# Kernel optimization log

Hardware: AMD Instinct MI355X
Metric: run time of the kernel (lower is better)

## Reference

```python
import jax, jax.numpy as jnp
import numpy as np

# Shapes: n groups, l = max group length, d = d_h, N = total queries (nq.sum()).
N_Q, N_GRP, L, D = 4096, 256, 64, 512


def setup_inputs() -> dict:
    key = jax.random.key(0)
    ks = jax.random.split(key, 8)
    q = jax.random.normal(ks[0], (N_Q, 2 * D), dtype=jnp.float32)      # cat([h_src, h_dst])
    k = jax.random.normal(ks[1], (N_GRP, L, D), dtype=jnp.float32)      # h_grp
    v = jax.random.normal(ks[2], (N_GRP, L, D), dtype=jnp.float32)      # x_grp
    m = (jax.random.uniform(ks[3], (N_GRP, L)) > 0.2).astype(jnp.float32)
    # sorted group id per query == repeat_interleave(arange(n), nq)
    gid = jnp.sort(jax.random.randint(ks[4], (N_Q,), 0, N_GRP))
    Wq = jax.random.normal(ks[5], (2 * D, D), dtype=jnp.float32) / np.float32(np.sqrt(2 * D))
    bq = jnp.zeros((D,), dtype=jnp.float32)
    Wk = jax.random.normal(ks[6], (D, D), dtype=jnp.float32) / np.float32(np.sqrt(D))
    bk = jnp.zeros((D,), dtype=jnp.float32)
    return dict(q=q, k=k, v=v, m=m, gid=gid, Wq=Wq, bq=bq, Wk=Wk, bk=bk)


def reference(q, k, v, m, gid, Wq, bq, Wk, bk):
    """Faithful jax version of NounPhraseModel.attention.

    torch: q -> self.q(q); k -> self.k(k); repeat_interleave(nq, 0) on k/v/m;
    s = (k @ q) / sqrt(d) - (exp(50*(1-m)) - 1); out = (v * softmax(s, 1)).sum(1).
    repeat_interleave is expressed as a gather by the per-query group id `gid`.
    """
    d = k.shape[-1]
    qp = q @ Wq + bq                                   # (N, d)   self.q(q)
    kp = k @ Wk + bk                                   # (n, l, d) self.k(k)
    kg = kp[gid]                                       # (N, l, d)
    vg = v[gid]                                        # (N, l, d)
    mg = m[gid]                                        # (N, l)
    s = jnp.einsum('nd,nld->nl', qp, kg) / jnp.sqrt(jnp.float32(d))
    s = s - (jnp.exp(50.0 * (1.0 - mg)) - 1.0)         # exponential mask bias
    a = jax.nn.softmax(s, axis=1)                      # softmax over group length
    return jnp.einsum('nl,nld->nd', a, vg)             # (N, d)
```

## Files before the change

### kernel.cpp

```cpp
#include <hip/hip_runtime.h>

#define NQ   4096
#define NGRP 256
#define LL   64
#define DD   512

typedef __attribute__((ext_vector_type(8))) short short8v;
typedef __attribute__((ext_vector_type(4))) float f32x4;
typedef __attribute__((ext_vector_type(4))) unsigned short us4v;

#define SCALE 0.044194173824159216f

static __device__ __forceinline__ unsigned short f2bf(float f) {
  union { float f; unsigned u; } x{f};
  unsigned r = x.u + 0x7fffu + ((x.u >> 16) & 1u);
  return (unsigned short)(r >> 16);
}
static __device__ __forceinline__ float bf2f(unsigned short h) {
  union { unsigned u; float f; } x{(unsigned)h << 16};
  return x.f;
}

static __device__ __forceinline__ void split_store(
    unsigned short* Hh, unsigned short* Hl, int r, int c4, float4 v) {
  int s = c4 >> 1, hf = c4 & 1;
  int base = (r * 8 + (s ^ (r & 7))) * 8 + hf * 4;
  unsigned short h0 = f2bf(v.x), h1 = f2bf(v.y), h2 = f2bf(v.z), h3 = f2bf(v.w);
  us4v hv = {h0, h1, h2, h3};
  us4v lv = {f2bf(v.x - bf2f(h0)), f2bf(v.y - bf2f(h1)),
             f2bf(v.z - bf2f(h2)), f2bf(v.w - bf2f(h3))};
  *(us4v*)(Hh + base) = hv;
  *(us4v*)(Hl + base) = lv;
}

static __device__ __forceinline__ short8v frag(const unsigned short* P, int r, int sl) {
  return *(const short8v*)(P + (r * 8 + (sl ^ (r & 7))) * 8);
}

__global__ __launch_bounds__(256) void k_prep(
    const float* __restrict__ q_in, const int* __restrict__ gid,
    const float* __restrict__ Wk, const float* __restrict__ Wq,
    const float* __restrict__ bq,
    unsigned short* __restrict__ qbf, int* __restrict__ starts,
    float* __restrict__ b2,
    unsigned short* __restrict__ w2t_h, unsigned short* __restrict__ w2t_l) {
  __shared__ __align__(16) unsigned short lds[4 * 64 * 64];
  int b = blockIdx.x, t = threadIdx.x;
  if (b < 128) {
    unsigned short* Ah = lds;
    unsigned short* Al = lds + 4096;
    unsigned short* Bh = lds + 8192;
    unsigned short* Bl = lds + 12288;
    int lane = t & 63, wid = t >> 6;
    int wm = wid >> 1, wn = wid & 1;
    int n0 = (b & 15) * 64, m0 = (b >> 4) * 64;
    f32x4 acc[2][2];
    #pragma unroll
    for (int i = 0; i < 2; ++i)
      #pragma unroll
      for (int j = 0; j < 2; ++j) acc[i][j] = (f32x4){0.f,0.f,0.f,0.f};

    for (int k0 = 0; k0 < 512; k0 += 64) {
      __syncthreads();
      #pragma unroll
      for (int i = 0; i < 4; ++i) {
        int idx = i * 256 + t, r = idx >> 4, c4 = idx & 15;
        float4 vA = *(const float4*)&Wk[(size_t)(m0 + r) * 512 + k0 + c4 * 4];
        split_store(Ah, Al, r, c4, vA);
        float4 vB = *(const float4*)&Wq[(size_t)(n0 + r) * 512 + k0 + c4 * 4];
        split_store(Bh, Bl, r, c4, vB);
      }
      __syncthreads();
      #pragma unroll
      for (int kk = 0; kk < 2; ++kk) {
        int sl = kk * 4 + (lane >> 4);
        short8v aH[2], aL[2], bH[2], bL[2];
        #pragma unroll
        for (int fm = 0; fm < 2; ++fm) {
          int r = wm * 32 + fm * 16 + (lane & 15);
          aH[fm] = frag(Ah, r, sl); aL[fm] = frag(Al, r, sl);
        }
        #pragma unroll
        for (int fn = 0; fn < 2; ++fn) {
          int r = wn * 32 + fn * 16 + (lane & 15);
          bH[fn] = frag(Bh, r, sl); bL[fn] = frag(Bl, r, sl);
        }
        #pragma unroll
        for (int fm = 0; fm < 2; ++fm)
          #pragma unroll
          for (int fn = 0; fn < 2; ++fn) {
            acc[fm][fn] = __builtin_amdgcn_mfma_f32_16x16x32_bf16(aH[fm], bH[fn], acc[fm][fn], 0, 0, 0);
            acc[fm][fn] = __builtin_amdgcn_mfma_f32_16x16x32_bf16(aH[fm], bL[fn], acc[fm][fn], 0, 0, 0);
            acc[fm][fn] = __builtin_amdgcn_mfma_f32_16x16x32_bf16(aL[fm], bH[fn], acc[fm][fn], 0, 0, 0);
          }
      }
    }
    int cn = lane & 15, rq = lane >> 4;
    #pragma unroll
    for (int fm = 0; fm < 2; ++fm)
      #pragma unroll
      for (int fn = 0; fn < 2; ++fn)
        #pragma unroll
        for (int j = 0; j < 4; ++j) {
          int m = m0 + wm * 32 + fm * 16 + rq * 4 + j;
          int n = n0 + wn * 32 + fn * 16 + cn;
          float c = acc[fm][fn][j];
          unsigned short hi = f2bf(c);
          unsigned short lo = f2bf(c - bf2f(hi));
          size_t off = (size_t)m * 1024 + n;
          w2t_h[off] = hi; w2t_l[off] = lo;
        }
  } else if (b < 2176) {
    int idx = (b - 128) * 256 + t;
    const float* src = q_in + (size_t)idx * 8;
    float4 f0 = *(const float4*)src;
    float4 f1 = *(const float4*)(src + 4);
    uint4 pk;
    pk.x = (unsigned)f2bf(f0.x) | ((unsigned)f2bf(f0.y) << 16);
    pk.y = (unsigned)f2bf(f0.z) | ((unsigned)f2bf(f0.w) << 16);
    pk.z = (unsigned)f2bf(f1.x) | ((unsigned)f2bf(f1.y) << 16);
    pk.w = (unsigned)f2bf(f1.z) | ((unsigned)f2bf(f1.w) << 16);
    ((uint4*)qbf)[idx] = pk;
  } else if (b == 2176) {
    for (int g = t; g <= NGRP; g += 256) {
      int lo = 0, hi = NQ;
      while (lo < hi) { int mid = (lo + hi) >> 1; if (gid[mid] < g) lo = mid + 1; else hi = mid; }
      starts[g] = lo;
    }
  } else {
    int dd = (b - 2177) * 256 + t;
    if (dd < DD) {
      float s = 0.f;
      const float* row = Wk + (size_t)dd * DD;
      for (int j = 0; j < DD; j += 4) {
        float4 w = *(const float4*)&row[j];
        float4 bb = *(const float4*)&bq[j];
        s += w.x*bb.x + w.y*bb.y + w.z*bb.z + w.w*bb.w;
      }
      b2[dd] = s;
    }
  }
}

__global__ __launch_bounds__(256) void gemm_qt_mfma(
    const unsigned short* __restrict__ qbf,
    const unsigned short* __restrict__ w2t_h,
    const unsigned short* __restrict__ w2t_l,
    const float* __restrict__ b2,
    unsigned short* __restrict__ qt_h, unsigned short* __restrict__ qt_l) {
  __shared__ __align__(16) unsigned short As[64 * 64];
  __shared__ __align__(16) unsigned short Bh[64 * 64];
  __shared__ __align__(16) unsigned short Bl[64 * 64];
  int t = threadIdx.x;
  int lane = t & 63, wid = t >> 6;
  int wm = wid >> 1, wn = wid & 1;
  int n0 = blockIdx.x * 64, m0 = blockIdx.y * 64;

  f32x4 acc[2][2];
  #pragma unroll
  for (int i = 0; i < 2; ++i)
    #pragma unroll
    for (int j = 0; j < 2; ++j) acc[i][j] = (f32x4){0.f, 0.f, 0.f, 0.f};

  for (int k0 = 0; k0 < 1024; k0 += 64) {
    __syncthreads();
    #pragma unroll
    for (int i = 0; i < 2; ++i) {
      int idx = i * 256 + t;
      int r = idx >> 3, s = idx & 7;
      int dst = r * 8 + (s ^ (r & 7));
      ((uint4*)As)[dst] = *(const uint4*)(qbf + (size_t)(m0 + r) * 1024 + k0 + s * 8);
    }
    #pragma unroll
    for (int i = 0; i < 2; ++i) {
      int idx = i * 256 + t;
      int r = idx >> 3, s = idx & 7;
      int dst = r * 8 + (s ^ (r & 7));
      ((uint4*)Bh)[dst] = *(const uint4*)(w2t_h + (size_t)(n0 + r) * 1024 + k0 + s * 8);
      ((uint4*)Bl)[dst] = *(const uint4*)(w2t_l + (size_t)(n0 + r) * 1024 + k0 + s * 8);
    }
    __syncthreads();
    #pragma unroll
    for (int kk = 0; kk < 2; ++kk) {
      short8v aF[2], bHF[2], bLF[2];
      int sl = kk * 4 + (lane >> 4);
      #pragma unroll
      for (int fm = 0; fm < 2; ++fm)
        aF[fm] = frag(As, wm * 32 + fm * 16 + (lane & 15), sl);
      #pragma unroll
      for (int fn = 0; fn < 2; ++fn) {
        int r = wn * 32 + fn * 16 + (lane & 15);
        bHF[fn] = frag(Bh, r, sl);
        bLF[fn] = frag(Bl, r, sl);
      }
      #pragma unroll
      for (int fm = 0; fm < 2; ++fm)
        #pragma unroll
        for (int fn = 0; fn < 2; ++fn) {
          acc[fm][fn] = __builtin_amdgcn_mfma_f32_16x16x32_bf16(aF[fm], bHF[fn], acc[fm][fn], 0, 0, 0);
          acc[fm][fn] = __builtin_amdgcn_mfma_f32_16x16x32_bf16(aF[fm], bLF[fn], acc[fm][fn], 0, 0, 0);
        }
    }
  }
  int cn = lane & 15, rq = lane >> 4;
  #pragma unroll
  for (int fn = 0; fn < 2; ++fn) {
    int n = n0 + wn * 32 + fn * 16 + cn;
    float bias = b2[n];
    #pragma unroll
    for (int fm = 0; fm < 2; ++fm)
      #pragma unroll
      for (int j = 0; j < 4; ++j) {
        int m = m0 + wm * 32 + fm * 16 + rq * 4 + j;
        float val = acc[fm][fn][j] + bias;
        unsigned short hi = f2bf(val);
        unsigned short lo = f2bf(val - bf2f(hi));
        qt_h[(size_t)m * 512 + n] = hi;
        qt_l[(size_t)m * 512 + n] = lo;
      }
  }
}

__global__ __launch_bounds__(256) void k_scores4(
    const unsigned short* __restrict__ qt_h, const unsigned short* __restrict__ qt_l,
    const float* __restrict__ kk_, const int* __restrict__ starts,
    float* __restrict__ s_part) {
  int g = blockIdx.x >> 2, dq = blockIdx.x & 3;
  int t = threadIdx.x, lane = t & 63, wl = t >> 6;
  int s0 = starts[g], s1 = starts[g + 1];
  if (s0 >= s1) return;

  __shared__ __align__(16) unsigned short Kh[64*64], Kl[64*64];
  __shared__ __align__(16) unsigned short Qh[32*64], Ql[32*64];

  float* sp = s_part + (size_t)dq * NQ * LL;

  for (int cs = s0; cs < s1; cs += 32) {
    int qc = min(32, s1 - cs);
    f32x4 acc[2];
    acc[0] = (f32x4){0.f,0.f,0.f,0.f};
    acc[1] = (f32x4){0.f,0.f,0.f,0.f};

    #pragma unroll
    for (int kt = 0; kt < 2; ++kt) {
      int k0 = dq * 128 + kt * 64;
      __syncthreads();
      #pragma unroll
      for (int i = 0; i < 4; ++i) {
        int idx = i * 256 + t, r = idx >> 4, c4 = idx & 15;
        float4 v = *(const float4*)&kk_[((size_t)g * LL + r) * DD + k0 + c4 * 4];
        split_store(Kh, Kl, r, c4, v);
      }
      {
        int r = t >> 3, s = t & 7;
        uint4 vh = make_uint4(0,0,0,0), vl = make_uint4(0,0,0,0);
        if (r < qc) {
          vh = *(const uint4*)&qt_h[(size_t)(cs + r) * DD + k0 + s * 8];
          vl = *(const uint4*)&qt_l[(size_t)(cs + r) * DD + k0 + s * 8];
        }
        int slot = r * 8 + (s ^ (r & 7));
        ((uint4*)Qh)[slot] = vh;
        ((uint4*)Ql)[slot] = vl;
      }
      __syncthreads();
      #pragma unroll
      for (int kk = 0; kk < 2; ++kk) {
        int sl = kk * 4 + (lane >> 4);
        int rA = wl * 16 + (lane & 15);
        short8v aH = frag(Kh, rA, sl), aL = frag(Kl, rA, sl);
        #pragma unroll
        for (int fn = 0; fn < 2; ++fn) {
          int rB = fn * 16 + (lane & 15);
          short8v bH = frag(Qh, rB, sl), bL = frag(Ql, rB, sl);
          acc[fn] = __builtin_amdgcn_mfma_f32_16x16x32_bf16(aH, bH, acc[fn], 0, 0, 0);
          acc[fn] = __builtin_amdgcn_mfma_f32_16x16x32_bf16(aH, bL, acc[fn], 0, 0, 0);
          acc[fn] = __builtin_amdgcn_mfma_f32_16x16x32_bf16(aL, bH, acc[fn], 0, 0, 0);
        }
      }
    }
    {
      int cq = lane & 15, rq = lane >> 4;
      #pragma unroll
      for (int fn = 0; fn < 2; ++fn) {
        int q = fn * 16 + cq;
        if (q < qc) {
          float* row = sp + (size_t)(cs + q) * LL;
          #pragma unroll
          for (int j = 0; j < 4; ++j)
            row[wl * 16 + rq * 4 + j] = acc[fn][j];
        }
      }
    }
  }
}

__global__ __launch_bounds__(256) void k_pv2(
    const float* __restrict__ s_part, const float* __restrict__ vv_,
    const float* __restrict__ msk, const int* __restrict__ starts,
    float* __restrict__ out) {
  int g = blockIdx.x >> 1, dh = blockIdx.x & 1;
  int t = threadIdx.x, lane = t & 63, wid = t >> 6;
  int s0 = starts[g], s1 = starts[g + 1];
  if (s0 >= s1) return;

  __shared__ __align__(16) float S_lds[32][68];
  __shared__ float bias_lds[LL];
  if (t < LL) bias_lds[t] = __expf(50.0f * (1.0f - msk[g * LL + t])) - 1.0f;

  const float* vb = vv_ + (size_t)g * LL * DD + dh * 256 + lane * 4;

  for (int cs = s0; cs < s1; cs += 32) {
    int qc = min(32, s1 - cs);
    __syncthreads();
    #pragma unroll
    for (int i = 0; i < 2; ++i) {
      int f = i * 256 + t;
      int q = f >> 4, l4 = f & 15;
      const float* p = s_part + (size_t)(cs + q) * LL + l4 * 4;
      float4 a0 = *(const float4*)p;
      float4 a1 = *(const float4*)(p + (size_t)NQ * LL);
      float4 a2 = *(const float4*)(p + (size_t)2 * NQ * LL);
      float4 a3 = *(const float4*)(p + (size_t)3 * NQ * LL);
      float4 r;
      r.x = (a0.x + a1.x + a2.x + a3.x) * SCALE - bias_lds[l4 * 4 + 0];
      r.y = (a0.y + a1.y + a2.y + a3.y) * SCALE - bias_lds[l4 * 4 + 1];
      r.z = (a0.z + a1.z + a2.z + a3.z) * SCALE - bias_lds[l4 * 4 + 2];
      r.w = (a0.w + a1.w + a2.w + a3.w) * SCALE - bias_lds[l4 * 4 + 3];
      *(float4*)&S_lds[q][l4 * 4] = r;
    }
    __syncthreads();
    {
      int q = t >> 3, i = t & 7;
      float4 x0 = *(const float4*)&S_lds[q][i * 8];
      float4 x1 = *(const float4*)&S_lds[q][i * 8 + 4];
      float mx = fmaxf(fmaxf(fmaxf(x0.x, x0.y), fmaxf(x0.z, x0.w)),
                       fmaxf(fmaxf(x1.x, x1.y), fmaxf(x1.z, x1.w)));
      #pragma unroll
      for (int off = 1; off < 8; off <<= 1) mx = fmaxf(mx, __shfl_xor(mx, off, 8));
      float e0 = __expf(x0.x - mx), e1 = __expf(x0.y - mx);
      float e2 = __expf(x0.z - mx), e3 = __expf(x0.w - mx);
      float e4 = __expf(x1.x - mx), e5 = __expf(x1.y - mx);
      float e6 = __expf(x1.z - mx), e7 = __expf(x1.w - mx);
      float sum = ((e0 + e1) + (e2 + e3)) + ((e4 + e5) + (e6 + e7));
      #pragma unroll
      for (int off = 1; off < 8; off <<= 1) sum += __shfl_xor(sum, off, 8);
      float inv = 1.0f / sum;
      *(float4*)&S_lds[q][i * 8]     = make_float4(e0 * inv, e1 * inv, e2 * inv, e3 * inv);
      *(float4*)&S_lds[q][i * 8 + 4] = make_float4(e4 * inv, e5 * inv, e6 * inv, e7 * inv);
    }
    __syncthreads();
    {
      float o[8][4];
      #pragma unroll
      for (int u = 0; u < 8; ++u)
        #pragma unroll
        for (int e = 0; e < 4; ++e) o[u][e] = 0.f;
      for (int l0 = 0; l0 < LL; l0 += 4) {
        float a_[8][4];
        #pragma unroll
        for (int u = 0; u < 8; ++u) {
          float4 av = *(const float4*)&S_lds[wid * 8 + u][l0];
          a_[u][0] = av.x; a_[u][1] = av.y; a_[u][2] = av.z; a_[u][3] = av.w;
        }
        #pragma unroll
        for (int e = 0; e < 4; ++e) {
          float4 vv = *(const float4*)&vb[(size_t)(l0 + e) * DD];
          #pragma unroll
          for (int u = 0; u < 8; ++u) {
            o[u][0] += a_[u][e] * vv.x;
            o[u][1] += a_[u][e] * vv.y;
            o[u][2] += a_[u][e] * vv.z;
            o[u][3] += a_[u][e] * vv.w;
          }
        }
      }
      #pragma unroll
      for (int u = 0; u < 8; ++u) {
        int q = wid * 8 + u;
        if (q < qc) {
          *(float4*)&out[(size_t)(cs + q) * DD + dh * 256 + lane * 4] =
              make_float4(o[u][0], o[u][1], o[u][2], o[u][3]);
        }
      }
    }
  }
}

extern "C" void kernel_launch(void* const* d_in, const int* in_sizes, int n_in,
                              void* d_out, int out_size, void* d_ws, size_t ws_size,
                              hipStream_t stream) {
  const float* q_in = (const float*)d_in[0];
  const float* k_in = (const float*)d_in[1];
  const float* v_in = (const float*)d_in[2];
  const float* m_in = (const float*)d_in[3];
  const int*   gid  = (const int*)d_in[4];
  const float* Wq   = (const float*)d_in[5];
  const float* bq   = (const float*)d_in[6];
  const float* Wk   = (const float*)d_in[7];
  float* out = (float*)d_out;

  unsigned short* w2t_h = (unsigned short*)d_ws;
  unsigned short* w2t_l = w2t_h + 512 * 1024;
  unsigned short* qt_h  = w2t_l + 512 * 1024;
  unsigned short* qt_l  = qt_h + 4096 * 512;
  unsigned short* qbf   = qt_l + 4096 * 512;
  float* b2 = (float*)(qbf + 4096 * 1024);
  int* starts = (int*)(b2 + 512);
  float* s_part = (float*)(starts + 512);

  k_prep<<<2179, 256, 0, stream>>>(q_in, gid, Wk, Wq, bq, qbf, starts, b2, w2t_h, w2t_l);
  gemm_qt_mfma<<<dim3(8, 64), 256, 0, stream>>>(qbf, w2t_h, w2t_l, b2, qt_h, qt_l);
  k_scores4<<<NGRP * 4, 256, 0, stream>>>(qt_h, qt_l, k_in, starts, s_part);
  k_pv2<<<NGRP * 2, 256, 0, stream>>>(s_part, v_in, m_in, starts, out);
}
```

Before: 70.27 us.

## Drop hi/lo bf16 split for fused weight and projected queries; retile weight GEMM

```diff
diff --git a/kernel.cpp b/kernel.cpp
--- a/kernel.cpp
+++ b/kernel.cpp
@@ -42,28 +42,24 @@
     const float* __restrict__ Wk, const float* __restrict__ Wq,
     const float* __restrict__ bq,
     unsigned short* __restrict__ qbf, int* __restrict__ starts,
-    float* __restrict__ b2,
-    unsigned short* __restrict__ w2t_h, unsigned short* __restrict__ w2t_l) {
-  __shared__ __align__(16) unsigned short lds[4 * 64 * 64];
+    float* __restrict__ b2, unsigned short* __restrict__ w2t) {
+  __shared__ __align__(16) unsigned short lds[4 * 32 * 64];
   int b = blockIdx.x, t = threadIdx.x;
-  if (b < 128) {
+  if (b < 512) {
     unsigned short* Ah = lds;
-    unsigned short* Al = lds + 4096;
-    unsigned short* Bh = lds + 8192;
-    unsigned short* Bl = lds + 12288;
+    unsigned short* Al = lds + 2048;
+    unsigned short* Bh = lds + 4096;
+    unsigned short* Bl = lds + 6144;
     int lane = t & 63, wid = t >> 6;
     int wm = wid >> 1, wn = wid & 1;
-    int n0 = (b & 15) * 64, m0 = (b >> 4) * 64;
-    f32x4 acc[2][2];
-    #pragma unroll
-    for (int i = 0; i < 2; ++i)
-      #pragma unroll
-      for (int j = 0; j < 2; ++j) acc[i][j] = (f32x4){0.f,0.f,0.f,0.f};
+    int m0 = (b >> 5) * 32;
+    int n0 = (b & 31) * 32;
+    f32x4 acc = (f32x4){0.f, 0.f, 0.f, 0.f};
 
     for (int k0 = 0; k0 < 512; k0 += 64) {
       __syncthreads();
       #pragma unroll
-      for (int i = 0; i < 4; ++i) {
+      for (int i = 0; i < 2; ++i) {
         int idx = i * 256 + t, r = idx >> 4, c4 = idx & 15;
         float4 vA = *(const float4*)&Wk[(size_t)(m0 + r) * 512 + k0 + c4 * 4];
         split_store(Ah, Al, r, c4, vA);
@@ -74,44 +70,24 @@
       #pragma unroll
       for (int kk = 0; kk < 2; ++kk) {
         int sl = kk * 4 + (lane >> 4);
-        short8v aH[2], aL[2], bH[2], bL[2];
-        #pragma unroll
-        for (int fm = 0; fm < 2; ++fm) {
-          int r = wm * 32 + fm * 16 + (lane & 15);
-          aH[fm] = frag(Ah, r, sl); aL[fm] = frag(Al, r, sl);
-        }
-        #pragma unroll
-        for (int fn = 0; fn < 2; ++fn) {
-          int r = wn * 32 + fn * 16 + (lane & 15);
-          bH[fn] = frag(Bh, r, sl); bL[fn] = frag(Bl, r, sl);
-        }
-        #pragma unroll
-        for (int fm = 0; fm < 2; ++fm)
-          #pragma unroll
-          for (int fn = 0; fn < 2; ++fn) {
-            acc[fm][fn] = __builtin_amdgcn_mfma_f32_16x16x32_bf16(aH[fm], bH[fn], acc[fm][fn], 0, 0, 0);
-            acc[fm][fn] = __builtin_amdgcn_mfma_f32_16x16x32_bf16(aH[fm], bL[fn], acc[fm][fn], 0, 0, 0);
-            acc[fm][fn] = __builtin_amdgcn_mfma_f32_16x16x32_bf16(aL[fm], bH[fn], acc[fm][fn], 0, 0, 0);
-          }
+        int rA = wm * 16 + (lane & 15);
+        int rB = wn * 16 + (lane & 15);
+        short8v aH = frag(Ah, rA, sl), aL = frag(Al, rA, sl);
+        short8v bH = frag(Bh, rB, sl), bL = frag(Bl, rB, sl);
+        acc = __builtin_amdgcn_mfma_f32_16x16x32_bf16(aH, bH, acc, 0, 0, 0);
+        acc = __builtin_amdgcn_mfma_f32_16x16x32_bf16(aH, bL, acc, 0, 0, 0);
+        acc = __builtin_amdgcn_mfma_f32_16x16x32_bf16(aL, bH, acc, 0, 0, 0);
       }
     }
     int cn = lane & 15, rq = lane >> 4;
     #pragma unroll
-    for (int fm = 0; fm < 2; ++fm)
-      #pragma unroll
-      for (int fn = 0; fn < 2; ++fn)
-        #pragma unroll
-        for (int j = 0; j < 4; ++j) {
-          int m = m0 + wm * 32 + fm * 16 + rq * 4 + j;
-          int n = n0 + wn * 32 + fn * 16 + cn;
-          float c = acc[fm][fn][j];
-          unsigned short hi = f2bf(c);
-          unsigned short lo = f2bf(c - bf2f(hi));
-          size_t off = (size_t)m * 1024 + n;
-          w2t_h[off] = hi; w2t_l[off] = lo;
-        }
-  } else if (b < 2176) {
-    int idx = (b - 128) * 256 + t;
+    for (int j = 0; j < 4; ++j) {
+      int m = m0 + wm * 16 + rq * 4 + j;
+      int n = n0 + wn * 16 + cn;
+      w2t[(size_t)m * 1024 + n] = f2bf(acc[j]);
+    }
+  } else if (b < 2560) {
+    int idx = (b - 512) * 256 + t;
     const float* src = q_in + (size_t)idx * 8;
     float4 f0 = *(const float4*)src;
     float4 f1 = *(const float4*)(src + 4);
@@ -121,14 +97,14 @@
     pk.z = (unsigned)f2bf(f1.x) | ((unsigned)f2bf(f1.y) << 16);
     pk.w = (unsigned)f2bf(f1.z) | ((unsigned)f2bf(f1.w) << 16);
     ((uint4*)qbf)[idx] = pk;
-  } else if (b == 2176) {
+  } else if (b == 2560) {
     for (int g = t; g <= NGRP; g += 256) {
       int lo = 0, hi = NQ;
       while (lo < hi) { int mid = (lo + hi) >> 1; if (gid[mid] < g) lo = mid + 1; else hi = mid; }
       starts[g] = lo;
     }
   } else {
-    int dd = (b - 2177) * 256 + t;
+    int dd = (b - 2561) * 256 + t;
     if (dd < DD) {
       float s = 0.f;
       const float* row = Wk + (size_t)dd * DD;
@@ -144,13 +120,11 @@
 
 __global__ __launch_bounds__(256) void gemm_qt_mfma(
     const unsigned short* __restrict__ qbf,
-    const unsigned short* __restrict__ w2t_h,
-    const unsigned short* __restrict__ w2t_l,
+    const unsigned short* __restrict__ w2t,
     const float* __restrict__ b2,
-    unsigned short* __restrict__ qt_h, unsigned short* __restrict__ qt_l) {
+    unsigned short* __restrict__ qt) {
   __shared__ __align__(16) unsigned short As[64 * 64];
-  __shared__ __align__(16) unsigned short Bh[64 * 64];
-  __shared__ __align__(16) unsigned short Bl[64 * 64];
+  __shared__ __align__(16) unsigned short Bs[64 * 64];
   int t = threadIdx.x;
   int lane = t & 63, wid = t >> 6;
   int wm = wid >> 1, wn = wid & 1;
@@ -170,36 +144,24 @@
       int r = idx >> 3, s = idx & 7;
       int dst = r * 8 + (s ^ (r & 7));
       ((uint4*)As)[dst] = *(const uint4*)(qbf + (size_t)(m0 + r) * 1024 + k0 + s * 8);
-    }
-    #pragma unroll
-    for (int i = 0; i < 2; ++i) {
-      int idx = i * 256 + t;
-      int r = idx >> 3, s = idx & 7;
-      int dst = r * 8 + (s ^ (r & 7));
-      ((uint4*)Bh)[dst] = *(const uint4*)(w2t_h + (size_t)(n0 + r) * 1024 + k0 + s * 8);
-      ((uint4*)Bl)[dst] = *(const uint4*)(w2t_l + (size_t)(n0 + r) * 1024 + k0 + s * 8);
+      ((uint4*)Bs)[dst] = *(const uint4*)(w2t + (size_t)(n0 + r) * 1024 + k0 + s * 8);
     }
     __syncthreads();
     #pragma unroll
     for (int kk = 0; kk < 2; ++kk) {
-      short8v aF[2], bHF[2], bLF[2];
+      short8v aF[2], bF[2];
       int sl = kk * 4 + (lane >> 4);
       #pragma unroll
       for (int fm = 0; fm < 2; ++fm)
         aF[fm] = frag(As, wm * 32 + fm * 16 + (lane & 15), sl);
       #pragma unroll
-      for (int fn = 0; fn < 2; ++fn) {
-        int r = wn * 32 + fn * 16 + (lane & 15);
-        bHF[fn] = frag(Bh, r, sl);
-        bLF[fn] = frag(Bl, r, sl);
-      }
+      for (int fn = 0; fn < 2; ++fn)
+        bF[fn] = frag(Bs, wn * 32 + fn * 16 + (lane & 15), sl);
       #pragma unroll
       for (int fm = 0; fm < 2; ++fm)
         #pragma unroll
-        for (int fn = 0; fn < 2; ++fn) {
-          acc[fm][fn] = __builtin_amdgcn_mfma_f32_16x16x32_bf16(aF[fm], bHF[fn], acc[fm][fn], 0, 0, 0);
-          acc[fm][fn] = __builtin_amdgcn_mfma_f32_16x16x32_bf16(aF[fm], bLF[fn], acc[fm][fn], 0, 0, 0);
-        }
+        for (int fn = 0; fn < 2; ++fn)
+          acc[fm][fn] = __builtin_amdgcn_mfma_f32_16x16x32_bf16(aF[fm], bF[fn], acc[fm][fn], 0, 0, 0);
     }
   }
   int cn = lane & 15, rq = lane >> 4;
@@ -212,17 +174,13 @@
       #pragma unroll
       for (int j = 0; j < 4; ++j) {
         int m = m0 + wm * 32 + fm * 16 + rq * 4 + j;
-        float val = acc[fm][fn][j] + bias;
-        unsigned short hi = f2bf(val);
-        unsigned short lo = f2bf(val - bf2f(hi));
-        qt_h[(size_t)m * 512 + n] = hi;
-        qt_l[(size_t)m * 512 + n] = lo;
+        qt[(size_t)m * 512 + n] = f2bf(acc[fm][fn][j] + bias);
       }
   }
 }
 
 __global__ __launch_bounds__(256) void k_scores4(
-    const unsigned short* __restrict__ qt_h, const unsigned short* __restrict__ qt_l,
+    const unsigned short* __restrict__ qt,
     const float* __restrict__ kk_, const int* __restrict__ starts,
     float* __restrict__ s_part) {
   int g = blockIdx.x >> 2, dq = blockIdx.x & 3;
@@ -231,7 +189,7 @@
   if (s0 >= s1) return;
 
   __shared__ __align__(16) unsigned short Kh[64*64], Kl[64*64];
-  __shared__ __align__(16) unsigned short Qh[32*64], Ql[32*64];
+  __shared__ __align__(16) unsigned short Qs[32*64];
 
   float* sp = s_part + (size_t)dq * NQ * LL;
 
@@ -253,14 +211,9 @@
       }
       {
         int r = t >> 3, s = t & 7;
-        uint4 vh = make_uint4(0,0,0,0), vl = make_uint4(0,0,0,0);
-        if (r < qc) {
-          vh = *(const uint4*)&qt_h[(size_t)(cs + r) * DD + k0 + s * 8];
-          vl = *(const uint4*)&qt_l[(size_t)(cs + r) * DD + k0 + s * 8];
-        }
-        int slot = r * 8 + (s ^ (r & 7));
-        ((uint4*)Qh)[slot] = vh;
-        ((uint4*)Ql)[slot] = vl;
+        uint4 vh = make_uint4(0,0,0,0);
+        if (r < qc) vh = *(const uint4*)&qt[(size_t)(cs + r) * DD + k0 + s * 8];
+        ((uint4*)Qs)[r * 8 + (s ^ (r & 7))] = vh;
       }
       __syncthreads();
       #pragma unroll
@@ -270,11 +223,9 @@
         short8v aH = frag(Kh, rA, sl), aL = frag(Kl, rA, sl);
         #pragma unroll
         for (int fn = 0; fn < 2; ++fn) {
-          int rB = fn * 16 + (lane & 15);
-          short8v bH = frag(Qh, rB, sl), bL = frag(Ql, rB, sl);
-          acc[fn] = __builtin_amdgcn_mfma_f32_16x16x32_bf16(aH, bH, acc[fn], 0, 0, 0);
-          acc[fn] = __builtin_amdgcn_mfma_f32_16x16x32_bf16(aH, bL, acc[fn], 0, 0, 0);
-          acc[fn] = __builtin_amdgcn_mfma_f32_16x16x32_bf16(aL, bH, acc[fn], 0, 0, 0);
+          short8v bF = frag(Qs, fn * 16 + (lane & 15), sl);
+          acc[fn] = __builtin_amdgcn_mfma_f32_16x16x32_bf16(aH, bF, acc[fn], 0, 0, 0);
+          acc[fn] = __builtin_amdgcn_mfma_f32_16x16x32_bf16(aL, bF, acc[fn], 0, 0, 0);
         }
       }
     }
@@ -399,17 +350,15 @@
   const float* Wk   = (const float*)d_in[7];
   float* out = (float*)d_out;
 
-  unsigned short* w2t_h = (unsigned short*)d_ws;
-  unsigned short* w2t_l = w2t_h + 512 * 1024;
-  unsigned short* qt_h  = w2t_l + 512 * 1024;
-  unsigned short* qt_l  = qt_h + 4096 * 512;
-  unsigned short* qbf   = qt_l + 4096 * 512;
+  unsigned short* w2t = (unsigned short*)d_ws;
+  unsigned short* qt  = w2t + 512 * 1024;
+  unsigned short* qbf = qt + 4096 * 512;
   float* b2 = (float*)(qbf + 4096 * 1024);
   int* starts = (int*)(b2 + 512);
   float* s_part = (float*)(starts + 512);
 
-  k_prep<<<2179, 256, 0, stream>>>(q_in, gid, Wk, Wq, bq, qbf, starts, b2, w2t_h, w2t_l);
-  gemm_qt_mfma<<<dim3(8, 64), 256, 0, stream>>>(qbf, w2t_h, w2t_l, b2, qt_h, qt_l);
-  k_scores4<<<NGRP * 4, 256, 0, stream>>>(qt_h, qt_l, k_in, starts, s_part);
+  k_prep<<<2563, 256, 0, stream>>>(q_in, gid, Wk, Wq, bq, qbf, starts, b2, w2t);
+  gemm_qt_mfma<<<dim3(8, 64), 256, 0, stream>>>(qbf, w2t, b2, qt);
+  k_scores4<<<NGRP * 4, 256, 0, stream>>>(qt, k_in, starts, s_part);
   k_pv2<<<NGRP * 2, 256, 0, stream>>>(s_part, v_in, m_in, starts, out);
 }
```

After: 79.35 us. +12.9%, slower.
